# Kernel optimization log

Hardware: AMD Instinct MI355X
Metric: run time of the kernel (lower is better)

Reference implementation:

```python
import jax, jax.numpy as jnp
import numpy as np

C = 192   # channels (class attr)
N = 196   # tokens per stream; 2N = 392, R feat dim = 784
B = 256

def _pw(x, w, b):
    # 1x1 Conv1d == pointwise channel mix: x [B,Ci,L] -> [B,Co,L]
    return jnp.einsum('oi,bil->bol', w, x) + b[None, :, None]

def _bn(x, g, beta, m, v):
    # eval-mode BatchNorm1d
    inv = g / jnp.sqrt(v + 1e-5)
    return (x - m[None, :, None]) * inv[None, :, None] + beta[None, :, None]

def setup_inputs():
    key = jax.random.key(0)
    ks = jax.random.split(key, 24)
    s = 1.0 / np.sqrt(C)
    d = {}
    d['x'] = jax.random.normal(ks[0], (B, N, C), dtype=jnp.float32)
    d['y'] = jax.random.normal(ks[1], (B, N, C), dtype=jnp.float32)
    # linear_conv_1: Conv1d(C,C,1) + BN + ReLU
    d['w1'] = jax.random.normal(ks[2], (C, C), dtype=jnp.float32) * s
    d['b1'] = jax.random.normal(ks[3], (C,), dtype=jnp.float32) * 0.01
    d['g1'] = jnp.ones((C,), jnp.float32)
    d['be1'] = jnp.zeros((C,), jnp.float32)
    d['m1'] = jax.random.normal(ks[4], (C,), dtype=jnp.float32) * 0.1
    d['v1'] = jax.random.uniform(ks[5], (C,), dtype=jnp.float32) + 0.5
    # linear_conv_2
    d['w2'] = jax.random.normal(ks[6], (C, C), dtype=jnp.float32) * s
    d['b2'] = jax.random.normal(ks[7], (C,), dtype=jnp.float32) * 0.01
    d['g2'] = jnp.ones((C,), jnp.float32)
    d['be2'] = jnp.zeros((C,), jnp.float32)
    d['m2'] = jax.random.normal(ks[8], (C,), dtype=jnp.float32) * 0.1
    d['v2'] = jax.random.uniform(ks[9], (C,), dtype=jnp.float32) + 0.5
    # linear_conv_3: Conv1d(C,C,1)
    d['w3'] = jax.random.normal(ks[10], (C, C), dtype=jnp.float32) * s
    d['b3'] = jax.random.normal(ks[11], (C,), dtype=jnp.float32) * 0.01
    # linear_conv_4: Conv1d(784,784,1)
    d['w4'] = jax.random.normal(ks[12], (784, 784), dtype=jnp.float32) / np.sqrt(784)
    d['b4'] = jax.random.normal(ks[13], (784,), dtype=jnp.float32) * 0.01
    # linear_conv_5: Conv1d(C+784,1,1)
    d['w5'] = jax.random.normal(ks[14], (1, C + 784), dtype=jnp.float32) / np.sqrt(C + 784)
    d['b5'] = jax.random.normal(ks[15], (1,), dtype=jnp.float32) * 0.01
    return d

def reference(x, y, w1, b1, g1, be1, m1, v1, w2, b2, g2, be2, m2, v2, w3, b3, w4, b4, w5, b5):
    xp = jnp.swapaxes(x, 1, 2)  # [B,C,N]
    yp = jnp.swapaxes(y, 1, 2)
    phi_x = jax.nn.relu(_bn(_pw(xp, w1, b1), g1, be1, m1, v1))
    phi_y = jax.nn.relu(_bn(_pw(yp, w2, b2), g2, be2, m2, v2))
    cat_phi = jnp.concatenate([phi_x, phi_y], axis=2)            # [B,C,2N]
    A = jnp.einsum('bcn,bcm->bnm', cat_phi, cat_phi)             # [B,2N,2N]
    # R[b,i,:] = cat(A[b,i,:], A[b,:,i]) for i in 0..2N-1, then permute(0,2,1)
    R = jnp.concatenate([A, jnp.swapaxes(A, 1, 2)], axis=2)      # [B,2N,4N]
    R = jnp.swapaxes(R, 1, 2)                                    # [B,4N,2N] = [B,784,392]
    v = _pw(cat_phi, w3, b3)                                     # [B,C,392]
    v_ = _pw(R, w4, b4)                                          # [B,784,392]
    cat_v = jnp.concatenate([v, v_], axis=1)                     # [B,976,392]
    W = _pw(cat_v, w5, b5)                                       # [B,1,392]
    out = xp * W[:, :, :N] + yp * W[:, :, N:]                    # [B,C,N]
    return out
```

## Files before the change

kernel.cpp:

```cpp
#include <hip/hip_runtime.h>
#include <hip/hip_bf16.h>

typedef __attribute__((ext_vector_type(8))) short bf16x8;
typedef __attribute__((ext_vector_type(4))) float f32x4;

#define CDIM 192
#define NTOK 196
#define LTOT 392
#define BDIM 256
#define NBE 64

__device__ __forceinline__ ushort f2bf(float f) {
  uint u = __float_as_uint(f);
  u = (u + 0x7FFFu + ((u >> 16) & 1u)) >> 16;
  return (ushort)u;
}
__device__ __forceinline__ float bf2f(ushort h) {
  return __uint_as_float(((uint)h) << 16);
}
__device__ __forceinline__ uint pk2(float lo, float hi) {
  __hip_bfloat162 t = __float22bfloat162_rn(float2{lo, hi});
  uint r;
  __builtin_memcpy(&r, &t, 4);
  return r;
}
__device__ __forceinline__ float wave_reduce(float a) {
#pragma unroll
  for (int off = 32; off > 0; off >>= 1) a += __shfl_xor(a, off);
  return a;
}

__global__ __launch_bounds__(256) void prep_kernel(
    const float* __restrict__ w1, const float* __restrict__ b1, const float* __restrict__ g1,
    const float* __restrict__ be1, const float* __restrict__ m1, const float* __restrict__ v1,
    const float* __restrict__ w2, const float* __restrict__ b2, const float* __restrict__ g2,
    const float* __restrict__ be2, const float* __restrict__ m2, const float* __restrict__ v2,
    const float* __restrict__ w3, const float* __restrict__ b3,
    const float* __restrict__ w4, const float* __restrict__ b4,
    const float* __restrict__ w5, const float* __restrict__ b5,
    ushort* __restrict__ w1b, ushort* __restrict__ w2b,
    float* __restrict__ u3, float* __restrict__ u4, float* __restrict__ cvecs,
    float* __restrict__ Kc, float* __restrict__ s) {
  const int bid = blockIdx.x;
  const int wid = threadIdx.x >> 6, lane = threadIdx.x & 63;
  if (bid < NBE) {
    for (int i = bid * BDIM + threadIdx.x; i < 123264; i += NBE * BDIM) {
      if (i < 36864) {
        int o = i / CDIM;
        float inv = g1[o] * rsqrtf(v1[o] + 1e-5f);
        w1b[i] = f2bf(w1[i] * inv);
      } else if (i < 73728) {
        int j = i - 36864; int o = j / CDIM;
        float inv = g2[o] * rsqrtf(v2[o] + 1e-5f);
        w2b[j] = f2bf(w2[j] * inv);
      } else if (i < 74112) {
        int k = i - 73728; int h = k / CDIM, o = k % CDIM;
        const float* bb = h ? b2 : b1; const float* gg = h ? g2 : g1;
        const float* bee = h ? be2 : be1;
        const float* mm = h ? m2 : m1; const float* vv = h ? v2 : v1;
        float inv = gg[o] * rsqrtf(vv[o] + 1e-5f);
        cvecs[k] = (bb[o] - mm[o]) * inv + bee[o];
      } else {
        s[i - 74112] = 0.f;
      }
    }
  } else if (bid < NBE + 48) {
    int j = (bid - NBE) * 4 + wid;
    float a = 0.f;
    for (int c = lane; c < CDIM; c += 64) a += w5[c] * w3[c * CDIM + j];
    a = wave_reduce(a);
    if (lane == 0) u3[j] = a;
  } else if (bid < NBE + 48 + 98) {
    int j = (bid - NBE - 48) * 4 + wid;
    float a = 0.f;
    for (int o = lane; o < 784; o += 64)
      a += w5[CDIM + o] * (w4[o * 784 + j] + w4[o * 784 + j + LTOT]);
    a = wave_reduce(a);
    if (lane == 0) u4[j] = a;
  } else {
    if (wid == 0) {
      float a = 0.f;
      for (int i = lane; i < CDIM + 784; i += 64)
        a += (i < CDIM) ? w5[i] * b3[i] : w5[i] * b4[i - CDIM];
      a = wave_reduce(a);
      if (lane == 0) Kc[0] = a + b5[0];
    }
  }
}

__global__ __launch_bounds__(256) void phi_kernel(
    const float* __restrict__ x, const float* __restrict__ y,
    const ushort* __restrict__ w1b, const ushort* __restrict__ w2b,
    const float* __restrict__ cvecs, const float* __restrict__ u4,
    ushort* __restrict__ phiT, float* __restrict__ s) {
  const int bh = blockIdx.x, b = bh >> 1, h = bh & 1;
  const float* __restrict__ src = (h ? y : x) + (size_t)b * NTOK * CDIM;
  const ushort* __restrict__ wb = h ? w2b : w1b;
  __shared__ ushort Abuf[2][64 * CDIM];
  __shared__ float u4s[208];
  __shared__ float cs[CDIM];
  const int tid = threadIdx.x;
  for (int i = tid; i < 208; i += BDIM) u4s[i] = (i < NTOK) ? u4[h * NTOK + i] : 0.f;
  for (int i = tid; i < CDIM; i += BDIM) cs[i] = cvecs[h * CDIM + i];

  const int wid = tid >> 6, lane = tid & 63;
  const int lrow = lane & 15, kgrp = lane >> 4;
  const int cbase = wid * 48 + lrow;

  bf16x8 bfr[3][6];
#pragma unroll
  for (int ct = 0; ct < 3; ct++)
#pragma unroll
    for (int kk = 0; kk < 6; kk++)
      bfr[ct][kk] = *(const bf16x8*)(wb + (size_t)(cbase + ct * 16) * CDIM + kk * 32 + kgrp * 8);
  __syncthreads();
  const float csr[3] = {cs[cbase], cs[cbase + 16], cs[cbase + 32]};

  const float4* src4 = (const float4*)src;
  const int NF4 = NTOK * CDIM / 4;
  float sp[3] = {0.f, 0.f, 0.f};

  float4 pf[12];
#pragma unroll
  for (int p = 0; p < 12; p++) {
    pf[p] = src4[p * 256 + tid];
  }

  for (int r = 0; r < 4; r++) {
    ushort* Ab = &Abuf[r & 1][0];
#pragma unroll
    for (int p = 0; p < 12; p++) {
      const int fi = r * 3072 + p * 256 + tid;
      const int e = fi * 4;
      const int row = e / CDIM;
      const int col = e - row * CDIM;
      const int rl = row & 63;
      uint2 wv;
      if (fi < NF4) { wv.x = pk2(pf[p].x, pf[p].y); wv.y = pk2(pf[p].z, pf[p].w); }
      else          { wv.x = 0u; wv.y = 0u; }
      uint addr = (uint)(rl * (CDIM * 2) + col * 2);
      addr ^= (uint)((rl & 7) << 4);
      *(uint2*)((char*)Ab + addr) = wv;
    }
    if (r < 3) {
#pragma unroll
      for (int p = 0; p < 12; p++) {
        const int fi = (r + 1) * 3072 + p * 256 + tid;
        pf[p] = (fi < NF4) ? src4[fi] : float4{0.f, 0.f, 0.f, 0.f};
      }
    }
    __syncthreads();
#pragma unroll
    for (int tt = 0; tt < 4; tt++) {
      const int l0 = r * 64 + tt * 16;
      if (l0 < NTOK) {
        bf16x8 afr[6];
#pragma unroll
        for (int kk = 0; kk < 6; kk++) {
          uint addr = (uint)((tt * 16 + lrow) * (CDIM * 2) + (kk * 32 + kgrp * 8) * 2);
          addr ^= (uint)((lrow & 7) << 4);
          afr[kk] = *(const bf16x8*)((const char*)Ab + addr);
        }
        f32x4 acc0 = {0.f,0.f,0.f,0.f}, acc1 = {0.f,0.f,0.f,0.f}, acc2 = {0.f,0.f,0.f,0.f};
#pragma unroll
        for (int kk = 0; kk < 6; kk++) {
          acc0 = __builtin_amdgcn_mfma_f32_16x16x32_bf16(afr[kk], bfr[0][kk], acc0, 0, 0, 0);
          acc1 = __builtin_amdgcn_mfma_f32_16x16x32_bf16(afr[kk], bfr[1][kk], acc1, 0, 0, 0);
          acc2 = __builtin_amdgcn_mfma_f32_16x16x32_bf16(afr[kk], bfr[2][kk], acc2, 0, 0, 0);
        }
        const int lbase = l0 + 4 * kgrp;
        const float4 u4v = *(const float4*)&u4s[lbase];
        ushort* pT = phiT + ((size_t)b * LTOT + h * NTOK + lbase) * CDIM + cbase;
        auto epi = [&](const f32x4& acc, int ct, float& spc) {
          const float v0 = fmaxf(acc[0] + csr[ct], 0.f);
          const float v1 = fmaxf(acc[1] + csr[ct], 0.f);
          const float v2 = fmaxf(acc[2] + csr[ct], 0.f);
          const float v3 = fmaxf(acc[3] + csr[ct], 0.f);
          const uint p01 = pk2(v0, v1), p23 = pk2(v2, v3);
          ushort* q = pT + ct * 16;
          if (lbase + 0 < NTOK) q[0 * CDIM] = (ushort)p01;
          if (lbase + 1 < NTOK) q[1 * CDIM] = (ushort)(p01 >> 16);
          if (lbase + 2 < NTOK) q[2 * CDIM] = (ushort)p23;
          if (lbase + 3 < NTOK) q[3 * CDIM] = (ushort)(p23 >> 16);
          spc += u4v.x * v0 + u4v.y * v1 + u4v.z * v2 + u4v.w * v3;
        };
        epi(acc0, 0, sp[0]); epi(acc1, 1, sp[1]); epi(acc2, 2, sp[2]);
      }
    }
  }
#pragma unroll
  for (int ct = 0; ct < 3; ct++) {
    float v = sp[ct];
    v += __shfl_xor(v, 16);
    v += __shfl_xor(v, 32);
    if (kgrp == 0) atomicAdd(&s[b * CDIM + cbase + ct * 16], v);
  }
}

__global__ __launch_bounds__(256) void w_kernel(
    const ushort* __restrict__ phiT, const float* __restrict__ s,
    const float* __restrict__ u3, const float* __restrict__ Kc,
    float* __restrict__ W) {
  const int b = blockIdx.x / 7, sl = blockIdx.x % 7;
  __shared__ float coeff[CDIM];
  for (int i = threadIdx.x; i < CDIM; i += BDIM) coeff[i] = u3[i] + s[b * CDIM + i];
  __syncthreads();
  const int wid = threadIdx.x >> 6, lane = threadIdx.x & 63;
  const int lrow = lane & 15, lsub = lane >> 4;
  const float Kv = Kc[0];
  const int start = sl * 56;
  for (int base = start + wid * 4; base < start + 56; base += 16) {
    const int l = base + lsub;
    const ushort* p = phiT + ((size_t)b * LTOT + l) * CDIM;
    float acc = 0.f;
#pragma unroll
    for (int q = 0; q < 3; q++) {
      const int c = q * 64 + lrow * 4;
      ushort4 v = *(const ushort4*)(p + c);
      acc += coeff[c] * bf2f(v.x) + coeff[c + 1] * bf2f(v.y) +
             coeff[c + 2] * bf2f(v.z) + coeff[c + 3] * bf2f(v.w);
    }
#pragma unroll
    for (int off = 8; off > 0; off >>= 1) acc += __shfl_xor(acc, off);
    if (lrow == 0) W[b * LTOT + l] = acc + Kv;
  }
}

__global__ __launch_bounds__(256) void out_kernel(
    const float* __restrict__ x, const float* __restrict__ y,
    const float* __restrict__ W, float* __restrict__ out) {
  const int bid = blockIdx.x;
  const int b = bid / 42, t = bid % 42;
  const int ct = t / 7, nt = t % 7;
  __shared__ float tile[32][33];
  const int c0 = ct * 32, n0 = nt * 32;
  {
    const int tx4 = threadIdx.x & 7, ny = threadIdx.x >> 3;
    const int n = n0 + ny;
    float4 v = {0.f, 0.f, 0.f, 0.f};
    if (n < NTOK) {
      const float wx = W[b * LTOT + n];
      const float wy = W[b * LTOT + NTOK + n];
      const size_t xi = ((size_t)b * NTOK + n) * CDIM + c0 + 4 * tx4;
      const float4 xv = *(const float4*)&x[xi];
      const float4 yv = *(const float4*)&y[xi];
      v = float4{xv.x * wx + yv.x * wy, xv.y * wx + yv.y * wy,
                 xv.z * wx + yv.z * wy, xv.w * wx + yv.w * wy};
    }
    tile[ny][4 * tx4 + 0] = v.x; tile[ny][4 * tx4 + 1] = v.y;
    tile[ny][4 * tx4 + 2] = v.z; tile[ny][4 * tx4 + 3] = v.w;
  }
  __syncthreads();
  {
    const int cq = threadIdx.x >> 3, nq = threadIdx.x & 7;
    const int nn = n0 + 4 * nq;
    if (nn < NTOK) {
      float4 o;
      o.x = tile[4 * nq + 0][cq]; o.y = tile[4 * nq + 1][cq];
      o.z = tile[4 * nq + 2][cq]; o.w = tile[4 * nq + 3][cq];
      *(float4*)&out[((size_t)b * CDIM + c0 + cq) * NTOK + nn] = o;
    }
  }
}

extern "C" void kernel_launch(void* const* d_in, const int* in_sizes, int n_in,
                              void* d_out, int out_size, void* d_ws, size_t ws_size,
                              hipStream_t stream) {
  const float* x   = (const float*)d_in[0];
  const float* y   = (const float*)d_in[1];
  const float* w1  = (const float*)d_in[2];
  const float* b1  = (const float*)d_in[3];
  const float* g1  = (const float*)d_in[4];
  const float* be1 = (const float*)d_in[5];
  const float* m1  = (const float*)d_in[6];
  const float* v1  = (const float*)d_in[7];
  const float* w2  = (const float*)d_in[8];
  const float* b2  = (const float*)d_in[9];
  const float* g2  = (const float*)d_in[10];
  const float* be2 = (const float*)d_in[11];
  const float* m2  = (const float*)d_in[12];
  const float* v2  = (const float*)d_in[13];
  const float* w3  = (const float*)d_in[14];
  const float* b3  = (const float*)d_in[15];
  const float* w4  = (const float*)d_in[16];
  const float* b4  = (const float*)d_in[17];
  const float* w5  = (const float*)d_in[18];
  const float* b5  = (const float*)d_in[19];
  float* out = (float*)d_out;

  char* ws = (char*)d_ws;
  ushort* w1b  = (ushort*)ws;
  ushort* w2b  = (ushort*)(ws + 73728);
  float* fbase = (float*)(ws + 147456);
  float* u3    = fbase;
  float* u4    = fbase + 192;
  float* cvecs = fbase + 584;
  float* Kc    = fbase + 968;
  float* s     = fbase + 976;
  float* W     = fbase + 50176;
  ushort* phiT = (ushort*)d_out;

  prep_kernel<<<211, BDIM, 0, stream>>>(w1, b1, g1, be1, m1, v1,
                                        w2, b2, g2, be2, m2, v2,
                                        w3, b3, w4, b4, w5, b5,
                                        w1b, w2b, u3, u4, cvecs, Kc, s);
  phi_kernel<<<512, BDIM, 0, stream>>>(x, y, w1b, w2b, cvecs, u4, phiT, s);
  w_kernel<<<256 * 7, BDIM, 0, stream>>>(phiT, s, u3, Kc, W);
  out_kernel<<<256 * 42, BDIM, 0, stream>>>(x, y, W, out);
}
```

Measured before the change: 68.11 us.

## Split phi kernel across token halves and fuse W and output kernels

The phi kernel now launches four blocks per batch (batch × stream × token half), so each block processes two 64-token chunks and the grid doubles for better occupancy. The W-reduction and output scaling/transposition kernels are fused into one kernel that computes W for a 28-token slice in shared memory and then writes the transposed output, removing the intermediate W buffer and a launch. phiT moves from the output buffer to workspace, because the fused kernel writes out while other blocks still read phiT. Risks include extra atomics on s, a larger shared tile, and duplicate weight-fragment loads per block.

```diff
diff --git a/kernel.cpp b/kernel.cpp
--- a/kernel.cpp
+++ b/kernel.cpp
@@ -93,7 +93,8 @@
     const ushort* __restrict__ w1b, const ushort* __restrict__ w2b,
     const float* __restrict__ cvecs, const float* __restrict__ u4,
     ushort* __restrict__ phiT, float* __restrict__ s) {
-  const int bh = blockIdx.x, b = bh >> 1, h = bh & 1;
+  const int bid = blockIdx.x;
+  const int b = bid >> 2, h = (bid >> 1) & 1, g = bid & 1;
   const float* __restrict__ src = (h ? y : x) + (size_t)b * NTOK * CDIM;
   const ushort* __restrict__ wb = h ? w2b : w1b;
   __shared__ ushort Abuf[2][64 * CDIM];
@@ -120,13 +121,15 @@
   const int NF4 = NTOK * CDIM / 4;
   float sp[3] = {0.f, 0.f, 0.f};
 
+  const int r0 = g * 2, r1 = r0 + 2;
   float4 pf[12];
 #pragma unroll
   for (int p = 0; p < 12; p++) {
-    pf[p] = src4[p * 256 + tid];
-  }
-
-  for (int r = 0; r < 4; r++) {
+    const int fi = r0 * 3072 + p * 256 + tid;
+    pf[p] = (fi < NF4) ? src4[fi] : float4{0.f, 0.f, 0.f, 0.f};
+  }
+
+  for (int r = r0; r < r1; r++) {
     ushort* Ab = &Abuf[r & 1][0];
 #pragma unroll
     for (int p = 0; p < 12; p++) {
@@ -142,7 +145,7 @@
       addr ^= (uint)((rl & 7) << 4);
       *(uint2*)((char*)Ab + addr) = wv;
     }
-    if (r < 3) {
+    if (r + 1 < r1) {
 #pragma unroll
       for (int p = 0; p < 12; p++) {
         const int fi = (r + 1) * 3072 + p * 256 + tid;
@@ -197,69 +200,56 @@
   }
 }
 
-__global__ __launch_bounds__(256) void w_kernel(
+__global__ __launch_bounds__(256) void wout_kernel(
+    const float* __restrict__ x, const float* __restrict__ y,
     const ushort* __restrict__ phiT, const float* __restrict__ s,
     const float* __restrict__ u3, const float* __restrict__ Kc,
-    float* __restrict__ W) {
-  const int b = blockIdx.x / 7, sl = blockIdx.x % 7;
+    float* __restrict__ out) {
+  const int bid = blockIdx.x;
+  const int b = bid / 7, nt = bid % 7;
+  const int n0 = nt * 28;
   __shared__ float coeff[CDIM];
-  for (int i = threadIdx.x; i < CDIM; i += BDIM) coeff[i] = u3[i] + s[b * CDIM + i];
-  __syncthreads();
-  const int wid = threadIdx.x >> 6, lane = threadIdx.x & 63;
-  const int lrow = lane & 15, lsub = lane >> 4;
-  const float Kv = Kc[0];
-  const int start = sl * 56;
-  for (int base = start + wid * 4; base < start + 56; base += 16) {
-    const int l = base + lsub;
-    const ushort* p = phiT + ((size_t)b * LTOT + l) * CDIM;
+  __shared__ float Wl[56];
+  __shared__ float tile[28][193];
+  const int tid = threadIdx.x;
+  for (int i = tid; i < CDIM; i += BDIM) coeff[i] = u3[i] + s[b * CDIM + i];
+  __syncthreads();
+  const int wv = tid >> 6, lane = tid & 63;
+  const int rloc = wv * 16 + (lane >> 2), g4 = lane & 3;
+  if (rloc < 56) {
+    const int lg = (rloc < 28) ? (n0 + rloc) : (NTOK + n0 + rloc - 28);
+    const ushort* p = phiT + ((size_t)b * LTOT + lg) * CDIM + g4 * 48;
     float acc = 0.f;
 #pragma unroll
-    for (int q = 0; q < 3; q++) {
-      const int c = q * 64 + lrow * 4;
-      ushort4 v = *(const ushort4*)(p + c);
-      acc += coeff[c] * bf2f(v.x) + coeff[c + 1] * bf2f(v.y) +
-             coeff[c + 2] * bf2f(v.z) + coeff[c + 3] * bf2f(v.w);
-    }
-#pragma unroll
-    for (int off = 8; off > 0; off >>= 1) acc += __shfl_xor(acc, off);
-    if (lrow == 0) W[b * LTOT + l] = acc + Kv;
-  }
-}
-
-__global__ __launch_bounds__(256) void out_kernel(
-    const float* __restrict__ x, const float* __restrict__ y,
-    const float* __restrict__ W, float* __restrict__ out) {
-  const int bid = blockIdx.x;
-  const int b = bid / 42, t = bid % 42;
-  const int ct = t / 7, nt = t % 7;
-  __shared__ float tile[32][33];
-  const int c0 = ct * 32, n0 = nt * 32;
-  {
-    const int tx4 = threadIdx.x & 7, ny = threadIdx.x >> 3;
-    const int n = n0 + ny;
-    float4 v = {0.f, 0.f, 0.f, 0.f};
-    if (n < NTOK) {
-      const float wx = W[b * LTOT + n];
-      const float wy = W[b * LTOT + NTOK + n];
-      const size_t xi = ((size_t)b * NTOK + n) * CDIM + c0 + 4 * tx4;
-      const float4 xv = *(const float4*)&x[xi];
-      const float4 yv = *(const float4*)&y[xi];
-      v = float4{xv.x * wx + yv.x * wy, xv.y * wx + yv.y * wy,
-                 xv.z * wx + yv.z * wy, xv.w * wx + yv.w * wy};
-    }
-    tile[ny][4 * tx4 + 0] = v.x; tile[ny][4 * tx4 + 1] = v.y;
-    tile[ny][4 * tx4 + 2] = v.z; tile[ny][4 * tx4 + 3] = v.w;
-  }
-  __syncthreads();
-  {
-    const int cq = threadIdx.x >> 3, nq = threadIdx.x & 7;
-    const int nn = n0 + 4 * nq;
-    if (nn < NTOK) {
-      float4 o;
-      o.x = tile[4 * nq + 0][cq]; o.y = tile[4 * nq + 1][cq];
-      o.z = tile[4 * nq + 2][cq]; o.w = tile[4 * nq + 3][cq];
-      *(float4*)&out[((size_t)b * CDIM + c0 + cq) * NTOK + nn] = o;
-    }
+    for (int q = 0; q < 12; q++) {
+      ushort4 v = *(const ushort4*)(p + q * 4);
+      const float* cf = &coeff[g4 * 48 + q * 4];
+      acc += cf[0] * bf2f(v.x) + cf[1] * bf2f(v.y) +
+             cf[2] * bf2f(v.z) + cf[3] * bf2f(v.w);
+    }
+    acc += __shfl_xor(acc, 1);
+    acc += __shfl_xor(acc, 2);
+    if (g4 == 0) Wl[rloc] = acc + Kc[0];
+  }
+  __syncthreads();
+  for (int i = tid; i < 28 * 48; i += BDIM) {
+    const int nl = i / 48, c4 = (i % 48) * 4;
+    const size_t xi = ((size_t)b * NTOK + n0 + nl) * CDIM + c4;
+    const float4 xv = *(const float4*)&x[xi];
+    const float4 yv = *(const float4*)&y[xi];
+    const float wx = Wl[nl], wy = Wl[28 + nl];
+    tile[nl][c4 + 0] = xv.x * wx + yv.x * wy;
+    tile[nl][c4 + 1] = xv.y * wx + yv.y * wy;
+    tile[nl][c4 + 2] = xv.z * wx + yv.z * wy;
+    tile[nl][c4 + 3] = xv.w * wx + yv.w * wy;
+  }
+  __syncthreads();
+  for (int i = tid; i < CDIM * 7; i += BDIM) {
+    const int c = i / 7, nq = i % 7;
+    float4 o;
+    o.x = tile[nq * 4 + 0][c]; o.y = tile[nq * 4 + 1][c];
+    o.z = tile[nq * 4 + 2][c]; o.w = tile[nq * 4 + 3][c];
+    *(float4*)&out[((size_t)b * CDIM + c) * NTOK + n0 + nq * 4] = o;
   }
 }
 
@@ -297,14 +287,12 @@
   float* cvecs = fbase + 584;
   float* Kc    = fbase + 968;
   float* s     = fbase + 976;
-  float* W     = fbase + 50176;
-  ushort* phiT = (ushort*)d_out;
+  ushort* phiT = (ushort*)(ws + (1 << 22));
 
   prep_kernel<<<211, BDIM, 0, stream>>>(w1, b1, g1, be1, m1, v1,
                                         w2, b2, g2, be2, m2, v2,
                                         w3, b3, w4, b4, w5, b5,
                                         w1b, w2b, u3, u4, cvecs, Kc, s);
-  phi_kernel<<<512, BDIM, 0, stream>>>(x, y, w1b, w2b, cvecs, u4, phiT, s);
-  w_kernel<<<256 * 7, BDIM, 0, stream>>>(phiT, s, u3, Kc, W);
-  out_kernel<<<256 * 42, BDIM, 0, stream>>>(x, y, W, out);
-}
+  phi_kernel<<<1024, BDIM, 0, stream>>>(x, y, w1b, w2b, cvecs, u4, phiT, s);
+  wout_kernel<<<256 * 7, BDIM, 0, stream>>>(x, y, phiT, s, u3, Kc, out);
+}
```

Result: no change. 68.72 us (+0.9%).
